# Performance work log

Measured on AMD Instinct MI355X. Metric: run time of the kernel, lower is better.

The kernel has to match this reference:

```python
import jax, jax.numpy as jnp
import numpy as np

DEPTH = 3  # weights are SHARED across depth (same module object repeated in ModuleList)


def prelu(x, a):
    # nn.PReLU() with a single shared slope parameter
    return jnp.where(x >= 0, x, a * x)


def conv1x1(x, w, b):
    # x: (N,C,H,W), w: (O,C), b: (O,)
    return jnp.einsum('nchw,oc->nohw', x, w) + b[None, :, None, None]


def conv3x3(x, w, b):
    # w: (O,I,3,3), padding=1 stride=1 -> SAME
    y = jax.lax.conv_general_dilated(x, w, (1, 1), 'SAME',
                                     dimension_numbers=('NCHW', 'OIHW', 'NCHW'))
    return y + b[None, :, None, None]


def _unit(x, w1, b1, a1, w2, b2, a2, w3, b3, a3, wc, bc):
    # NonLocalAttention
    e1 = prelu(conv1x1(x, w1, b1), a1)   # (N,C,H,W)
    e2 = prelu(conv1x1(x, w2, b2), a2)   # (N,C,H,W)
    asm = prelu(conv1x1(x, w3, b3), a3)  # (N,C,H,W)
    N, C, H, W = e1.shape
    q = e1.reshape(N, C, H * W).transpose(0, 2, 1)     # (N,HW,C)
    k = e2.reshape(N, C, H * W)                        # (N,C,HW)
    score = jax.nn.softmax(jnp.matmul(q, k), axis=2)   # (N,HW,HW)
    v = asm.reshape(N, C, H * W).transpose(0, 2, 1)    # (N,HW,C)
    att = jnp.matmul(score, v).transpose(0, 2, 1).reshape(N, C, H, W)
    # Conv2d(channel, channel, 3, 1, 1) + exact GELU
    return jax.nn.gelu(conv3x3(att, wc, bc), approximate=False)


def setup_inputs() -> dict:
    key = jax.random.key(0)
    ks = jax.random.split(key, 8)
    C = 128
    x = jax.random.normal(ks[0], (1, C, 96, 96), dtype=jnp.float32)
    s = 0.05
    inp = {
        'x': x,
        'w1': jax.random.normal(ks[1], (C, C), jnp.float32) * s,
        'b1': jnp.zeros((C,), jnp.float32),
        'a1': jnp.float32(0.25),
        'w2': jax.random.normal(ks[2], (C, C), jnp.float32) * s,
        'b2': jnp.zeros((C,), jnp.float32),
        'a2': jnp.float32(0.25),
        'w3': jax.random.normal(ks[3], (C, C), jnp.float32) * s,
        'b3': jnp.zeros((C,), jnp.float32),
        'a3': jnp.float32(0.25),
        'wc': jax.random.normal(ks[4], (C, C, 3, 3), jnp.float32) * s,
        'bc': jnp.zeros((C,), jnp.float32),
    }
    return inp


def reference(x, w1, b1, a1, w2, b2, a2, w3, b3, a3, wc, bc):
    res = x
    for _ in range(DEPTH):  # same (shared) weights each iteration, per original module
        res = _unit(res, w1, b1, a1, w2, b2, a2, w3, b3, a3, wc, bc)
    return x + res
```

## Files before the change

### kernel.cpp

```cpp
#include <hip/hip_runtime.h>

#define HWPX 9216
#define NCH  128

typedef float  f32x4  __attribute__((ext_vector_type(4)));
typedef __bf16 bf16x8 __attribute__((ext_vector_type(8)));
typedef __bf16 bf16x4 __attribute__((ext_vector_type(4)));

#define SWZ16(row) ((((row) & 7) ^ (((row) >> 3) << 1)) << 4)

#define DPP_MAX(v)                                                             \
  do {                                                                         \
    v = fmaxf(v, __int_as_float(__builtin_amdgcn_update_dpp(                   \
               0, __float_as_int(v), 0xB1, 0xF, 0xF, true)));                  \
    v = fmaxf(v, __int_as_float(__builtin_amdgcn_update_dpp(                   \
               0, __float_as_int(v), 0x4E, 0xF, 0xF, true)));                  \
    v = fmaxf(v, __int_as_float(__builtin_amdgcn_update_dpp(                   \
               0, __float_as_int(v), 0x124, 0xF, 0xF, true)));                 \
    v = fmaxf(v, __int_as_float(__builtin_amdgcn_update_dpp(                   \
               0, __float_as_int(v), 0x128, 0xF, 0xF, true)));                 \
  } while (0)

__global__ __launch_bounds__(256) void prep_kernel(
    const float* __restrict__ w1, const float* __restrict__ w2,
    const float* __restrict__ w3, const float* __restrict__ wc,
    const float* __restrict__ x,
    __bf16* __restrict__ Wb, __bf16* __restrict__ wck,
    __bf16* __restrict__ Xb) {
  int tid = blockIdx.x * 256 + threadIdx.x;
  int nt  = gridDim.x * 256;
  for (int idx = tid; idx < 3 * 16384; idx += nt) {
    int j = idx >> 14;
    const float* w = (j == 0) ? w1 : (j == 1 ? w2 : w3);
    Wb[idx] = (__bf16)w[idx & 16383];
  }
  for (int idx = tid; idx < 147456; idx += nt) {
    int k = idx % 9;
    int rest = idx / 9;
    int c = rest & 127, o = rest >> 7;
    wck[(k * 128 + o) * 128 + c] = (__bf16)wc[idx];
  }
  for (int idx = tid; idx < 128 * HWPX; idx += nt) {
    int c = idx / HWPX, p = idx - c * HWPX;
    Xb[p * 128 + c] = (__bf16)x[idx];
  }
}

__global__ __launch_bounds__(256) void conv1x1_qkv(
    const __bf16* __restrict__ Xb, const __bf16* __restrict__ Wb,
    const float* __restrict__ b1, const float* __restrict__ b2,
    const float* __restrict__ b3, const float* __restrict__ a1,
    const float* __restrict__ a2, const float* __restrict__ a3,
    __bf16* __restrict__ Q, __bf16* __restrict__ K, __bf16* __restrict__ Vt) {
  const int tid = threadIdx.x, lane = tid & 63, w = tid >> 6;
  const int l16 = lane & 15, hi = lane >> 4;
  const int p0 = blockIdx.x * 64;
  const int z  = blockIdx.y;

  bf16x8 af[4][4];
#pragma unroll
  for (int pxt = 0; pxt < 4; ++pxt)
#pragma unroll
    for (int kc = 0; kc < 4; ++kc)
      af[pxt][kc] = *(const bf16x8*)&Xb[(p0 + pxt * 16 + l16) * 128 + kc * 32 + hi * 8];

  const int obase = w * 96 + z * 16;
  const int j = obase >> 7;
  const int oo = (obase & 127) + l16;
  bf16x8 bfg[4];
#pragma unroll
  for (int kc = 0; kc < 4; ++kc)
    bfg[kc] = *(const bf16x8*)&Wb[(obase + l16) * 128 + kc * 32 + hi * 8];
  f32x4 acc[4];
#pragma unroll
  for (int pxt = 0; pxt < 4; ++pxt) acc[pxt] = (f32x4){0.f, 0.f, 0.f, 0.f};
#pragma unroll
  for (int kc = 0; kc < 4; ++kc)
#pragma unroll
    for (int pxt = 0; pxt < 4; ++pxt)
      acc[pxt] = __builtin_amdgcn_mfma_f32_16x16x32_bf16(af[pxt][kc], bfg[kc], acc[pxt], 0, 0, 0);

  const float* bp = (j == 0) ? b1 : (j == 1 ? b2 : b3);
  const float bias = bp[oo];
  const float* ap = (j == 0) ? a1 : (j == 1 ? a2 : a3);
  const float sl = ap[0];
#pragma unroll
  for (int pxt = 0; pxt < 4; ++pxt)
#pragma unroll
    for (int r = 0; r < 4; ++r) {
      float v = acc[pxt][r] + bias;
      v = (v >= 0.f) ? v : sl * v;
      int px = p0 + pxt * 16 + hi * 4 + r;
      if (j == 0)      Q[px * 128 + oo] = (__bf16)(v * 1.44269504088896f);
      else if (j == 1) K[px * 128 + oo] = (__bf16)v;
      else             Vt[oo * HWPX + px] = (__bf16)v;
    }
}

__global__ __launch_bounds__(512) void flash_attn(
    const __bf16* __restrict__ Q, const __bf16* __restrict__ Kb,
    const __bf16* __restrict__ Vt, float* __restrict__ Opart,
    float* __restrict__ mOut, float* __restrict__ lOut, int nt) {
  __shared__ __align__(16) unsigned char smem[81920];
  const int tid  = threadIdx.x;
  const int lane = tid & 63;
  const int w    = tid >> 6;
  const int l16  = lane & 15;
  const int hi   = lane >> 4;
  const int ord  = blockIdx.y * 72 + blockIdx.x;
  const int nsp  = gridDim.y;
  const int split = ord % nsp;
  const int qb   = (ord / nsp) * 128;
  const int kt0  = split * nt;

  const __bf16* gsrc[4];
  unsigned loff[4];
  long gstep;
  if (w < 4) {
    gstep = 8192;
#pragma unroll
    for (int j = 0; j < 4; ++j) {
      int seg = w * 4 + j;
      int row = seg * 4 + (lane >> 4);
      int ch  = lane & 15;
      gsrc[j] = Kb + (size_t)(kt0 * 64 + row) * 128 + (ch ^ (row & 7)) * 8;
      loff[j] = seg * 1024;
    }
  } else {
    gstep = 64;
#pragma unroll
    for (int j = 0; j < 4; ++j) {
      int seg = (w - 4) * 4 + j;
      int d  = seg * 8 + (lane >> 3);
      int ch = lane & 7;
      gsrc[j] = Vt + (size_t)d * HWPX + kt0 * 64 + (ch ^ (d & 7)) * 8;
      loff[j] = 16384 + seg * 1024;
    }
  }

#define STAGE(BUF) do {                                                        \
  _Pragma("unroll")                                                            \
  for (int j = 0; j < 4; ++j) {                                                \
    __builtin_amdgcn_global_load_lds(                                          \
        (const __attribute__((address_space(1))) unsigned int*)gsrc[j],        \
        (__attribute__((address_space(3))) unsigned int*)(smem + (BUF) * 32768 \
                                                          + loff[j]),          \
        16, 0, 0);                                                             \
    gsrc[j] += gstep;                                                          \
  } } while (0)

  bf16x8 qf[4];
  const int qrow = qb + w * 16 + l16;
#pragma unroll
  for (int dc = 0; dc < 4; ++dc)
    qf[dc] = *(const bf16x8*)&Q[qrow * 128 + dc * 32 + hi * 8];

  bf16x8 ones;
#pragma unroll
  for (int e = 0; e < 8; ++e) ones[e] = (__bf16)1.0f;

  f32x4 oacc[8];
  f32x4 oacc_l = (f32x4){0.f, 0.f, 0.f, 0.f};
#pragma unroll
  for (int dc = 0; dc < 8; ++dc) oacc[dc] = (f32x4){0.f, 0.f, 0.f, 0.f};
  float m[4];
#pragma unroll
  for (int r = 0; r < 4; ++r) m[r] = -INFINITY;

  const unsigned pbase = 65536 + w * 2048;

  STAGE(0);
  __syncthreads();

  int cur = 0;
  for (int it = 0; it < nt; ++it) {
    if (it + 1 < nt) STAGE(cur ^ 1);

    const unsigned kb0 = cur * 32768;
    f32x4 s[4];
    __builtin_amdgcn_s_setprio(1);
#pragma unroll
    for (int g = 0; g < 4; ++g) {
      s[g] = (f32x4){0.f, 0.f, 0.f, 0.f};
      int row = g * 16 + l16;
#pragma unroll
      for (int dc = 0; dc < 4; ++dc) {
        bf16x8 kf = *(const bf16x8*)&smem[kb0 + row * 256 +
                        ((dc * 64 + hi * 16) ^ ((row & 7) << 4))];
        s[g] = __builtin_amdgcn_mfma_f32_16x16x32_bf16(qf[dc], kf, s[g], 0, 0, 0);
      }
    }
    __builtin_amdgcn_s_setprio(0);

    float mx[4];
#pragma unroll
    for (int r = 0; r < 4; ++r) {
      mx[r] = fmaxf(fmaxf(s[0][r], s[1][r]), fmaxf(s[2][r], s[3][r]));
      DPP_MAX(mx[r]);
    }
    bool need = false;
#pragma unroll
    for (int r = 0; r < 4; ++r) need = need || (mx[r] > m[r] + 8.f);
    if (__any(need)) {
#pragma unroll
      for (int r = 0; r < 4; ++r) {
        float mn = fmaxf(m[r], mx[r]);
        float alpha = __builtin_amdgcn_exp2f(m[r] - mn);
        m[r] = mn;
        oacc_l[r] *= alpha;
#pragma unroll
        for (int dc = 0; dc < 8; ++dc) oacc[dc][r] *= alpha;
      }
    }
#pragma unroll
    for (int g = 0; g < 4; ++g)
#pragma unroll
      for (int r = 0; r < 4; ++r) {
        int row = hi * 4 + r;
        *(__bf16*)&smem[pbase + row * 128 +
                        ((g * 32 + l16 * 2) ^ SWZ16(row))] =
            (__bf16)__builtin_amdgcn_exp2f(s[g][r] - m[r]);
      }
    bf16x8 pa[2];
#pragma unroll
    for (int kc = 0; kc < 2; ++kc)
      pa[kc] = *(const bf16x8*)&smem[pbase + l16 * 128 +
                   ((kc * 64 + hi * 16) ^ SWZ16(l16))];
    __builtin_amdgcn_s_setprio(1);
#pragma unroll
    for (int dc = 0; dc < 8; ++dc) {
#pragma unroll
      for (int kc = 0; kc < 2; ++kc) {
        int row = dc * 16 + l16;
        bf16x8 vf = *(const bf16x8*)&smem[kb0 + 16384 + row * 128 +
                        ((kc * 64 + hi * 16) ^ ((row & 7) << 4))];
        oacc[dc] = __builtin_amdgcn_mfma_f32_16x16x32_bf16(pa[kc], vf, oacc[dc], 0, 0, 0);
      }
    }
    oacc_l = __builtin_amdgcn_mfma_f32_16x16x32_bf16(pa[0], ones, oacc_l, 0, 0, 0);
    oacc_l = __builtin_amdgcn_mfma_f32_16x16x32_bf16(pa[1], ones, oacc_l, 0, 0, 0);
    __builtin_amdgcn_s_setprio(0);
    __syncthreads();
    cur ^= 1;
  }
#undef STAGE

  const int sbase = split * HWPX;
#pragma unroll
  for (int dc = 0; dc < 8; ++dc)
#pragma unroll
    for (int r = 0; r < 4; ++r) {
      int q = qb + w * 16 + hi * 4 + r;
      Opart[(size_t)(sbase + q) * 128 + dc * 16 + l16] = oacc[dc][r];
    }
  if (l16 == 0) {
#pragma unroll
    for (int r = 0; r < 4; ++r) {
      int q = qb + w * 16 + hi * 4 + r;
      mOut[sbase + q] = m[r];
      lOut[sbase + q] = oacc_l[r];
    }
  }
}

__global__ __launch_bounds__(256) void flash_combine(
    const float* __restrict__ Opart, const float* __restrict__ mArr,
    const float* __restrict__ lArr, __bf16* __restrict__ attb, int ksplit) {
  int idx = blockIdx.x * 256 + threadIdx.x;
  int q = idx >> 5, d4 = idx & 31;
  float M = -INFINITY;
  for (int i = 0; i < ksplit; ++i) M = fmaxf(M, mArr[i * HWPX + q]);
  float denom = 0.f;
  f32x4 acc = (f32x4){0.f, 0.f, 0.f, 0.f};
  for (int i = 0; i < ksplit; ++i) {
    float wi = __builtin_amdgcn_exp2f(mArr[i * HWPX + q] - M);
    denom += lArr[i * HWPX + q] * wi;
    f32x4 v = *(const f32x4*)&Opart[((size_t)i * HWPX + q) * 128 + d4 * 4];
#pragma unroll
    for (int e = 0; e < 4; ++e) acc[e] += wi * v[e];
  }
  float inv = 1.f / denom;
  bf16x4 r;
#pragma unroll
  for (int e = 0; e < 4; ++e) r[e] = (__bf16)(acc[e] * inv);
  *(bf16x4*)&attb[(size_t)q * 128 + d4 * 4] = r;
}

__global__ __launch_bounds__(256) void conv3x3_gelu(
    const __bf16* __restrict__ attb, const __bf16* __restrict__ wck,
    const float* __restrict__ bc, const float* __restrict__ resid,
    float* __restrict__ out, __bf16* __restrict__ xbo) {
  __shared__ __align__(16) unsigned char smem[26112];
  const int tid = threadIdx.x;
  const int y   = blockIdx.x / 3;
  const int x0  = (blockIdx.x % 3) * 32;
  const int oh  = blockIdx.y;
  const int lane = tid & 63, w = tid >> 6;
  const int l16 = lane & 15, hi = lane >> 4;

  for (int id = tid; id < 1632; id += 256) {
    int px = id >> 4, ch = id & 15;
    int hy = px / 34, hx = px - hy * 34;
    int gy = y + hy - 1, gx = x0 + hx - 1;
    bf16x8 v;
    if (gy >= 0 && gy < 96 && gx >= 0 && gx < 96) {
      v = *(const bf16x8*)&attb[(size_t)(gy * 96 + gx) * 128 + ch * 8];
    } else {
#pragma unroll
      for (int e = 0; e < 8; ++e) v[e] = (__bf16)0.f;
    }
    *(bf16x8*)&smem[px * 256 + ((ch * 16) ^ ((px & 7) << 4))] = v;
  }
  __syncthreads();

  const int ob = oh * 64 + w * 16;
  f32x4 acc[2];
#pragma unroll
  for (int pt = 0; pt < 2; ++pt)
#pragma unroll
    for (int r = 0; r < 4; ++r) acc[pt][r] = bc[ob + hi * 4 + r];

  for (int tap = 0; tap < 9; ++tap) {
    int dy = tap / 3, dx = tap - dy * 3;
#pragma unroll
    for (int cc = 0; cc < 4; ++cc) {
      bf16x8 af = *(const bf16x8*)&wck[(tap * 128 + ob + l16) * 128 +
                                       cc * 32 + hi * 8];
#pragma unroll
      for (int pt = 0; pt < 2; ++pt) {
        int px = dy * 34 + pt * 16 + l16 + dx;
        bf16x8 bf = *(const bf16x8*)&smem[px * 256 +
                        ((cc * 64 + hi * 16) ^ ((px & 7) << 4))];
        acc[pt] = __builtin_amdgcn_mfma_f32_16x16x32_bf16(af, bf, acc[pt], 0, 0, 0);
      }
    }
  }

  float ge[2][4];
#pragma unroll
  for (int pt = 0; pt < 2; ++pt)
#pragma unroll
    for (int r = 0; r < 4; ++r) {
      float v = acc[pt][r];
      ge[pt][r] = 0.5f * v * (1.f + erff(v * 0.70710678118654752f));
    }

  if (xbo) {
    __syncthreads();
#pragma unroll
    for (int pt = 0; pt < 2; ++pt)
#pragma unroll
      for (int r = 0; r < 4; ++r) {
        int oc = w * 16 + hi * 4 + r;
        int pl = pt * 16 + l16;
        *(__bf16*)&smem[pl * 256 + ((oc * 2) ^ ((pl & 7) << 4))] =
            (__bf16)ge[pt][r];
      }
    __syncthreads();
    for (int id = tid; id < 256; id += 256) {
      int pl = id >> 3, ch = id & 7;
      bf16x8 v = *(const bf16x8*)&smem[pl * 256 + ((ch * 16) ^ ((pl & 7) << 4))];
      *(bf16x8*)&xbo[(size_t)(y * 96 + x0 + pl) * 128 + oh * 64 + ch * 8] = v;
    }
  } else {
#pragma unroll
    for (int pt = 0; pt < 2; ++pt)
#pragma unroll
      for (int r = 0; r < 4; ++r) {
        int o  = ob + hi * 4 + r;
        int px = y * 96 + x0 + pt * 16 + l16;
        out[o * HWPX + px] = ge[pt][r] + resid[o * HWPX + px];
      }
  }
}

extern "C" void kernel_launch(void* const* d_in, const int* in_sizes, int n_in,
                              void* d_out, int out_size, void* d_ws, size_t ws_size,
                              hipStream_t stream) {
  const float* x  = (const float*)d_in[0];
  const float* w1 = (const float*)d_in[1];
  const float* b1 = (const float*)d_in[2];
  const float* a1 = (const float*)d_in[3];
  const float* w2 = (const float*)d_in[4];
  const float* b2 = (const float*)d_in[5];
  const float* a2 = (const float*)d_in[6];
  const float* w3 = (const float*)d_in[7];
  const float* b3 = (const float*)d_in[8];
  const float* a3 = (const float*)d_in[9];
  const float* wc = (const float*)d_in[10];
  const float* bc = (const float*)d_in[11];
  float* out = (float*)d_out;

  char* ws = (char*)d_ws;
  __bf16* attb = (__bf16*)(ws + 0);
  __bf16* Qb  = (__bf16*)(ws + 2359296);
  __bf16* Kb  = (__bf16*)(ws + 4718592);
  __bf16* Vt  = (__bf16*)(ws + 7077888);
  __bf16* Xb  = (__bf16*)(ws + 9437184);
  __bf16* Wb  = (__bf16*)(ws + 11796480);
  __bf16* wck = (__bf16*)(ws + 11894784);
  const size_t base_end = 12189696;

  int ksplit = 1;
  if (ws_size >= base_end + 8ull * (4718592 + 2 * 36864)) ksplit = 8;
  else if (ws_size >= base_end + 4ull * (4718592 + 2 * 36864)) ksplit = 4;
  else if (ws_size >= base_end + 2ull * (4718592 + 2 * 36864)) ksplit = 2;
  float* Opart = (float*)(ws + base_end);
  float* mArr  = (float*)(ws + base_end + (size_t)ksplit * 4718592);
  float* lArr  = (float*)(ws + base_end + (size_t)ksplit * (4718592 + 36864));

  prep_kernel<<<576, 256, 0, stream>>>(w1, w2, w3, wc, x, Wb, wck, Xb);

  for (int u = 0; u < 3; ++u) {
    conv1x1_qkv<<<dim3(144, 6), 256, 0, stream>>>(Xb, Wb, b1, b2, b3, a1, a2, a3,
                                                  Qb, Kb, Vt);
    flash_attn<<<dim3(72, ksplit), 512, 0, stream>>>(
        Qb, Kb, Vt, Opart, mArr, lArr, 144 / ksplit);
    flash_combine<<<1152, 256, 0, stream>>>(Opart, mArr, lArr, attb, ksplit);
    conv3x3_gelu<<<dim3(288, 2), 256, 0, stream>>>(attb, wck, bc,
                                                   (u == 2) ? x : nullptr,
                                                   (u == 2) ? out : nullptr,
                                                   (u < 2) ? Xb : nullptr);
  }
}
```

Measured before the change: 441.0 us.

## Store split-K attention partials in bf16, tile X transpose, merge conv3x3 halves

```diff
diff --git a/kernel.cpp b/kernel.cpp
--- a/kernel.cpp
+++ b/kernel.cpp
@@ -27,22 +27,42 @@
     const float* __restrict__ x,
     __bf16* __restrict__ Wb, __bf16* __restrict__ wck,
     __bf16* __restrict__ Xb) {
-  int tid = blockIdx.x * 256 + threadIdx.x;
-  int nt  = gridDim.x * 256;
-  for (int idx = tid; idx < 3 * 16384; idx += nt) {
-    int j = idx >> 14;
-    const float* w = (j == 0) ? w1 : (j == 1 ? w2 : w3);
-    Wb[idx] = (__bf16)w[idx & 16383];
-  }
-  for (int idx = tid; idx < 147456; idx += nt) {
-    int k = idx % 9;
-    int rest = idx / 9;
-    int c = rest & 127, o = rest >> 7;
-    wck[(k * 128 + o) * 128 + c] = (__bf16)wc[idx];
-  }
-  for (int idx = tid; idx < 128 * HWPX; idx += nt) {
-    int c = idx / HWPX, p = idx - c * HWPX;
-    Xb[p * 128 + c] = (__bf16)x[idx];
+  const int tid = threadIdx.x;
+  if (blockIdx.x < 144) {
+    __shared__ __bf16 xs[64][136];
+    const int p0 = blockIdx.x * 64;
+#pragma unroll
+    for (int i = 0; i < 8; ++i) {
+      int id = tid + i * 256;
+      int c = id >> 4, q4 = id & 15;
+      float4 v = *(const float4*)&x[c * HWPX + p0 + q4 * 4];
+      xs[q4 * 4 + 0][c] = (__bf16)v.x;
+      xs[q4 * 4 + 1][c] = (__bf16)v.y;
+      xs[q4 * 4 + 2][c] = (__bf16)v.z;
+      xs[q4 * 4 + 3][c] = (__bf16)v.w;
+    }
+    __syncthreads();
+#pragma unroll
+    for (int i = 0; i < 4; ++i) {
+      int id = tid + i * 256;
+      int px = id >> 4, ch = id & 15;
+      bf16x8 v = *(const bf16x8*)&xs[px][ch * 8];
+      *(bf16x8*)&Xb[(size_t)(p0 + px) * 128 + ch * 8] = v;
+    }
+  } else {
+    int base = (blockIdx.x - 144) * 256 + tid;
+    int nt = 16 * 256;
+    for (int idx = base; idx < 3 * 16384; idx += nt) {
+      int j = idx >> 14;
+      const float* w = (j == 0) ? w1 : (j == 1 ? w2 : w3);
+      Wb[idx] = (__bf16)w[idx & 16383];
+    }
+    for (int idx = base; idx < 147456; idx += nt) {
+      int k = idx % 9;
+      int rest = idx / 9;
+      int c = rest & 127, o = rest >> 7;
+      wck[(k * 128 + o) * 128 + c] = (__bf16)wc[idx];
+    }
   }
 }
 
@@ -99,7 +119,7 @@
 
 __global__ __launch_bounds__(512) void flash_attn(
     const __bf16* __restrict__ Q, const __bf16* __restrict__ Kb,
-    const __bf16* __restrict__ Vt, float* __restrict__ Opart,
+    const __bf16* __restrict__ Vt, __bf16* __restrict__ Opart,
     float* __restrict__ mOut, float* __restrict__ lOut, int nt) {
   __shared__ __align__(16) unsigned char smem[81920];
   const int tid  = threadIdx.x;
@@ -251,7 +271,7 @@
 #pragma unroll
     for (int r = 0; r < 4; ++r) {
       int q = qb + w * 16 + hi * 4 + r;
-      Opart[(size_t)(sbase + q) * 128 + dc * 16 + l16] = oacc[dc][r];
+      Opart[(size_t)(sbase + q) * 128 + dc * 16 + l16] = (__bf16)oacc[dc][r];
     }
   if (l16 == 0) {
 #pragma unroll
@@ -264,7 +284,7 @@
 }
 
 __global__ __launch_bounds__(256) void flash_combine(
-    const float* __restrict__ Opart, const float* __restrict__ mArr,
+    const __bf16* __restrict__ Opart, const float* __restrict__ mArr,
     const float* __restrict__ lArr, __bf16* __restrict__ attb, int ksplit) {
   int idx = blockIdx.x * 256 + threadIdx.x;
   int q = idx >> 5, d4 = idx & 31;
@@ -275,9 +295,9 @@
   for (int i = 0; i < ksplit; ++i) {
     float wi = __builtin_amdgcn_exp2f(mArr[i * HWPX + q] - M);
     denom += lArr[i * HWPX + q] * wi;
-    f32x4 v = *(const f32x4*)&Opart[((size_t)i * HWPX + q) * 128 + d4 * 4];
-#pragma unroll
-    for (int e = 0; e < 4; ++e) acc[e] += wi * v[e];
+    bf16x4 v = *(const bf16x4*)&Opart[((size_t)i * HWPX + q) * 128 + d4 * 4];
+#pragma unroll
+    for (int e = 0; e < 4; ++e) acc[e] += wi * (float)v[e];
   }
   float inv = 1.f / denom;
   bf16x4 r;
@@ -286,7 +306,7 @@
   *(bf16x4*)&attb[(size_t)q * 128 + d4 * 4] = r;
 }
 
-__global__ __launch_bounds__(256) void conv3x3_gelu(
+__global__ __launch_bounds__(512) void conv3x3_gelu(
     const __bf16* __restrict__ attb, const __bf16* __restrict__ wck,
     const float* __restrict__ bc, const float* __restrict__ resid,
     float* __restrict__ out, __bf16* __restrict__ xbo) {
@@ -294,11 +314,10 @@
   const int tid = threadIdx.x;
   const int y   = blockIdx.x / 3;
   const int x0  = (blockIdx.x % 3) * 32;
-  const int oh  = blockIdx.y;
   const int lane = tid & 63, w = tid >> 6;
   const int l16 = lane & 15, hi = lane >> 4;
 
-  for (int id = tid; id < 1632; id += 256) {
+  for (int id = tid; id < 1632; id += 512) {
     int px = id >> 4, ch = id & 15;
     int hy = px / 34, hx = px - hy * 34;
     int gy = y + hy - 1, gx = x0 + hx - 1;
@@ -313,7 +332,7 @@
   }
   __syncthreads();
 
-  const int ob = oh * 64 + w * 16;
+  const int ob = w * 16;
   f32x4 acc[2];
 #pragma unroll
   for (int pt = 0; pt < 2; ++pt)
@@ -351,16 +370,16 @@
     for (int pt = 0; pt < 2; ++pt)
 #pragma unroll
       for (int r = 0; r < 4; ++r) {
-        int oc = w * 16 + hi * 4 + r;
+        int oc = ob + hi * 4 + r;
         int pl = pt * 16 + l16;
         *(__bf16*)&smem[pl * 256 + ((oc * 2) ^ ((pl & 7) << 4))] =
             (__bf16)ge[pt][r];
       }
     __syncthreads();
-    for (int id = tid; id < 256; id += 256) {
-      int pl = id >> 3, ch = id & 7;
+    {
+      int pl = tid >> 4, ch = tid & 15;
       bf16x8 v = *(const bf16x8*)&smem[pl * 256 + ((ch * 16) ^ ((pl & 7) << 4))];
-      *(bf16x8*)&xbo[(size_t)(y * 96 + x0 + pl) * 128 + oh * 64 + ch * 8] = v;
+      *(bf16x8*)&xbo[(size_t)(y * 96 + x0 + pl) * 128 + ch * 8] = v;
     }
   } else {
 #pragma unroll
@@ -402,14 +421,14 @@
   const size_t base_end = 12189696;
 
   int ksplit = 1;
-  if (ws_size >= base_end + 8ull * (4718592 + 2 * 36864)) ksplit = 8;
-  else if (ws_size >= base_end + 4ull * (4718592 + 2 * 36864)) ksplit = 4;
-  else if (ws_size >= base_end + 2ull * (4718592 + 2 * 36864)) ksplit = 2;
-  float* Opart = (float*)(ws + base_end);
-  float* mArr  = (float*)(ws + base_end + (size_t)ksplit * 4718592);
-  float* lArr  = (float*)(ws + base_end + (size_t)ksplit * (4718592 + 36864));
-
-  prep_kernel<<<576, 256, 0, stream>>>(w1, w2, w3, wc, x, Wb, wck, Xb);
+  if (ws_size >= base_end + 8ull * (2359296 + 2 * 36864)) ksplit = 8;
+  else if (ws_size >= base_end + 4ull * (2359296 + 2 * 36864)) ksplit = 4;
+  else if (ws_size >= base_end + 2ull * (2359296 + 2 * 36864)) ksplit = 2;
+  __bf16* Opart = (__bf16*)(ws + base_end);
+  float* mArr  = (float*)(ws + base_end + (size_t)ksplit * 2359296);
+  float* lArr  = (float*)(ws + base_end + (size_t)ksplit * (2359296 + 36864));
+
+  prep_kernel<<<160, 256, 0, stream>>>(w1, w2, w3, wc, x, Wb, wck, Xb);
 
   for (int u = 0; u < 3; ++u) {
     conv1x1_qkv<<<dim3(144, 6), 256, 0, stream>>>(Xb, Wb, b1, b2, b3, a1, a2, a3,
@@ -417,9 +436,9 @@
     flash_attn<<<dim3(72, ksplit), 512, 0, stream>>>(
         Qb, Kb, Vt, Opart, mArr, lArr, 144 / ksplit);
     flash_combine<<<1152, 256, 0, stream>>>(Opart, mArr, lArr, attb, ksplit);
-    conv3x3_gelu<<<dim3(288, 2), 256, 0, stream>>>(attb, wck, bc,
-                                                   (u == 2) ? x : nullptr,
-                                                   (u == 2) ? out : nullptr,
-                                                   (u < 2) ? Xb : nullptr);
-  }
-}
+    conv3x3_gelu<<<288, 512, 0, stream>>>(attb, wck, bc,
+                                          (u == 2) ? x : nullptr,
+                                          (u == 2) ? out : nullptr,
+                                          (u < 2) ? Xb : nullptr);
+  }
+}
```

Result: no change. 448.9 us (+1.8%).
